# Performance work log

Measured on AMD Instinct MI355X. Metric: run time of the kernel, lower is better.

Reference implementation:

```python
import jax, jax.numpy as jnp
import numpy as np
import math

NUM_HEADS = 16
SEGMENT_SIZE = 256
DILATION_RATE = 2


def _hilbert_curve(n):
    if n == 1:
        return [(0, 0)]
    m = n // 2
    sub = _hilbert_curve(m)
    pts = [(y, x) for (x, y) in sub]
    pts += [(x, y + m) for (x, y) in sub]
    pts += [(x + m, y + m) for (x, y) in sub]
    pts += [(m - 1 - y + m, m - 1 - x) for (x, y) in sub]
    return pts


def generate_hilbert_curve_mapping(seq_len):
    grid = 2 ** int(math.ceil(math.log2(math.sqrt(seq_len))))
    pts = _hilbert_curve(grid)
    lin2hil = np.zeros(seq_len, dtype=np.int32)
    for h_idx, (x, y) in enumerate(pts[:seq_len]):
        lin = y * grid + x
        if lin < seq_len:
            lin2hil[lin] = h_idx
    return lin2hil


def setup_inputs() -> dict:
    key = jax.random.key(0)
    k1, k2, k3 = jax.random.split(key, 3)
    B, S, H = 1, 4096, 2048
    scale = H ** -0.5
    x = jax.random.normal(k1, (B, S, H), dtype=jnp.float32)
    w_qkv = jax.random.normal(k2, (3 * H, H), dtype=jnp.float32) * scale
    w_out = jax.random.normal(k3, (H, H), dtype=jnp.float32) * scale
    hilbert_map = jnp.asarray(generate_hilbert_curve_mapping(S))
    return {"x": x, "w_qkv": w_qkv, "w_out": w_out, "hilbert_map": hilbert_map}


def _kv_positions(S, seg, dil):
    # Union of per-segment dilated positions: seg_start + j*dil (< segment end).
    seg_starts = np.arange(0, S, seg)
    within = np.arange(0, seg, dil)
    return jnp.asarray((seg_starts[:, None] + within[None, :]).reshape(-1))


def reference(x, w_qkv, w_out, hilbert_map):
    B, S, H = x.shape
    nh = NUM_HEADS
    hd = H // nh
    qkv = x @ w_qkv.T                              # [B,S,3H]
    qkv = qkv.reshape(B, S, 3, nh, hd).transpose(2, 0, 3, 1, 4)  # [3,B,nh,S,hd]
    q, k, v = qkv[0], qkv[1], qkv[2]

    kv_pos = _kv_positions(S, SEGMENT_SIZE, DILATION_RATE)  # [Nk]
    gathered = hilbert_map[kv_pos]                 # Hilbert-mapped KV indices
    kg = k[:, :, gathered, :]                      # [B,nh,Nk,hd]
    vg = v[:, :, gathered, :]

    scale = 1.0 / jnp.sqrt(jnp.float32(hd))
    scores = jnp.einsum("bhmd,bhnd->bhmn", q, kg) * scale
    p = jax.nn.softmax(scores, axis=-1)
    acc = jnp.einsum("bhmn,bhnd->bhmd", p, vg)     # [B,nh,S,hd]

    # Scatter: out[:, :, hilbert_map[m], :] = acc[:, :, m, :]
    out = jnp.zeros_like(acc).at[:, :, hilbert_map, :].set(acc)
    out = out.transpose(0, 2, 1, 3).reshape(B, S, H)
    return out @ w_out.T
```

## Files before the change

kernel.cpp:

```cpp
#include <hip/hip_runtime.h>
#include <math.h>

#define S_LEN 4096
#define HID   2048
#define NH    16
#define HD    128
#define NKV   2048
#define KT    64
#define QBLK  256
#define NT    (NKV / KT)
#define QSCALE 0.12754103668587426f

typedef __attribute__((ext_vector_type(8))) _Float16 half8;
typedef __attribute__((ext_vector_type(4))) _Float16 half4;
typedef __attribute__((ext_vector_type(2))) __fp16 fp16x2;
typedef __attribute__((ext_vector_type(4))) float f32x4;
typedef __attribute__((ext_vector_type(16))) float f32x16;

#define GLB_AS __attribute__((address_space(1)))
#define LDS_AS __attribute__((address_space(3)))

#if __has_builtin(__builtin_amdgcn_exp2f)
#define EXP2(x) __builtin_amdgcn_exp2f(x)
#else
#define EXP2(x) exp2f(x)
#endif

__device__ __forceinline__ void gload16(const void* g, void* l) {
  __builtin_amdgcn_global_load_lds((GLB_AS const void*)g, (LDS_AS void*)l, 16, 0, 0);
}

__device__ __forceinline__ unsigned pkrtz(float a, float b) {
  union { fp16x2 h; unsigned u; } cv;
  cv.h = __builtin_amdgcn_cvt_pkrtz(a, b);
  return cv.u;
}

#define NX8  (S_LEN * HID / 8)
#define NW8  (3 * HID * HID / 8)
#define NO8  (HID * HID / 8)
__global__ void k_cvt_all(const float* __restrict__ x, const float* __restrict__ wq,
                          const float* __restrict__ wo, _Float16* __restrict__ x16,
                          _Float16* __restrict__ wq16, _Float16* __restrict__ wo16) {
  int i = blockIdx.x * 256 + threadIdx.x;
  const float* src; _Float16* dst; int j;
  if (i < NX8)            { src = x;  dst = x16;  j = i; }
  else if (i < NX8 + NW8) { src = wq; dst = wq16; j = i - NX8; }
  else                    { src = wo; dst = wo16; j = i - NX8 - NW8; }
  float4 a = ((const float4*)src)[2 * j];
  float4 b = ((const float4*)src)[2 * j + 1];
  half8 h;
  h[0] = (_Float16)a.x; h[1] = (_Float16)a.y; h[2] = (_Float16)a.z; h[3] = (_Float16)a.w;
  h[4] = (_Float16)b.x; h[5] = (_Float16)b.y; h[6] = (_Float16)b.z; h[7] = (_Float16)b.w;
  ((half8*)dst)[j] = h;
}

__global__ __launch_bounds__(512, 2)
void k_gemm_qkv8(const _Float16* __restrict__ A, const _Float16* __restrict__ wqkv,
                 _Float16* __restrict__ q16, const int* __restrict__ hmap,
                 char* __restrict__ kimg, char* __restrict__ vtimg)
{
  extern __shared__ __align__(16) char lds[];
  const int tid = threadIdx.x;
  const int w = tid >> 6, lane = tid & 63;
  const int l15 = lane & 15, l4 = lane >> 4;
  const int wr = w >> 2, wc = w & 3;
  const int K = HID;

  const int bid = (blockIdx.x & 7) * 32 + (blockIdx.x >> 3);
  const bool qpart = bid < 128;
  int m0, n0;
  const _Float16* B;
  if (qpart) { int b = bid;       m0 = (b >> 3) * 256; n0 = (b & 7) * 256;  B = wqkv; }
  else       { int b = bid - 128; m0 = (b >> 4) * 256; n0 = (b & 15) * 256; B = wqkv + (size_t)HID * HID; }

  const int r8 = lane >> 3;
  const int sl = (lane & 7) ^ r8;
  const _Float16* ApA[2][2];
  const _Float16* BpB[2][2];
#pragma unroll
  for (int mh = 0; mh < 2; ++mh)
#pragma unroll
    for (int L = 0; L < 2; ++L) {
      int rel = L * 128 + mh * 64 + w * 8 + r8;
      int grow = qpart ? (m0 + rel) : hmap[2 * (m0 + rel)];
      ApA[mh][L] = A + (size_t)grow * K + sl * 8;
    }
#pragma unroll
  for (int nh = 0; nh < 2; ++nh)
#pragma unroll
    for (int L = 0; L < 2; ++L) {
      int row = n0 + (L * 2 + (w >> 2)) * 64 + nh * 32 + (w & 3) * 8 + r8;
      BpB[nh][L] = B + (size_t)row * K + sl * 8;
    }

  const int sw0 = (l4 ^ (l15 & 7)) * 16;
  const int sw1 = ((4 + l4) ^ (l15 & 7)) * 16;
  const int rofs = l15 * 128;

  f32x4 acc[8][4];
#pragma unroll
  for (int i = 0; i < 8; ++i)
#pragma unroll
    for (int j = 0; j < 4; ++j) acc[i][j] = (f32x4){0.f, 0.f, 0.f, 0.f};
  half8 af[4][2], bf[2][2];

#define STG_A(MH, BUF, T)                                                       \
  do {                                                                          \
    gload16(ApA[MH][0] + (T) * 64, lds + (BUF)*65536 + (MH)*16384 + w * 1024);  \
    gload16(ApA[MH][1] + (T) * 64, lds + (BUF)*65536 + (MH)*16384 + 8192 + w * 1024); \
  } while (0)
#define STG_B(NH, BUF, T)                                                       \
  do {                                                                          \
    gload16(BpB[NH][0] + (T) * 64, lds + (BUF)*65536 + 32768 + (NH)*16384 + w * 1024); \
    gload16(BpB[NH][1] + (T) * 64, lds + (BUF)*65536 + 32768 + (NH)*16384 + 8192 + w * 1024); \
  } while (0)

#define PH(BUF, MH, NH, LA, LB, STG, WAITS)                                     \
  do {                                                                          \
    if (LA) {                                                                   \
      _Pragma("unroll")                                                         \
      for (int j = 0; j < 4; ++j) {                                             \
        af[j][0] = *(const half8*)(lds + (BUF)*65536 + (MH)*16384 + wr * 8192 + j * 2048 + rofs + sw0); \
        af[j][1] = *(const half8*)(lds + (BUF)*65536 + (MH)*16384 + wr * 8192 + j * 2048 + rofs + sw1); \
      }                                                                         \
    }                                                                           \
    if (LB) {                                                                   \
      _Pragma("unroll")                                                         \
      for (int jn = 0; jn < 2; ++jn) {                                          \
        bf[jn][0] = *(const half8*)(lds + (BUF)*65536 + 32768 + (NH)*16384 + wc * 4096 + jn * 2048 + rofs + sw0); \
        bf[jn][1] = *(const half8*)(lds + (BUF)*65536 + 32768 + (NH)*16384 + wc * 4096 + jn * 2048 + rofs + sw1); \
      }                                                                         \
    }                                                                           \
    STG;                                                                        \
    __builtin_amdgcn_s_barrier();                                               \
    __builtin_amdgcn_s_setprio(1);                                              \
    _Pragma("unroll")                                                           \
    for (int j = 0; j < 4; ++j)                                                 \
      _Pragma("unroll")                                                         \
      for (int jn = 0; jn < 2; ++jn)                                            \
        _Pragma("unroll")                                                       \
        for (int ks = 0; ks < 2; ++ks)                                          \
          acc[(MH)*4 + j][(NH)*2 + jn] = __builtin_amdgcn_mfma_f32_16x16x32_f16( \
              af[j][ks], bf[jn][ks], acc[(MH)*4 + j][(NH)*2 + jn], 0, 0, 0);    \
    __builtin_amdgcn_s_setprio(0);                                              \
    WAITS;                                                                      \
    __builtin_amdgcn_s_barrier();                                               \
  } while (0)

  STG_A(0, 0, 0); STG_B(1, 0, 0); STG_A(1, 0, 0); STG_B(0, 0, 0);
  STG_A(0, 1, 1); STG_B(1, 1, 1);
  asm volatile("s_waitcnt vmcnt(4)");
  __builtin_amdgcn_s_barrier();

  for (int i = 0; i < 15; ++i) {
    const int T1 = 2 * i + 1, T2 = 2 * i + 2, T3 = 2 * i + 3;
    PH(0, 0, 0, 1, 1, STG_A(1, 1, T1), (void)0);
    PH(0, 0, 1, 0, 1, STG_B(0, 1, T1), (void)0);
    PH(0, 1, 1, 1, 0, STG_A(0, 0, T2), (void)0);
    PH(0, 1, 0, 0, 1, STG_B(1, 0, T2), asm volatile("s_waitcnt vmcnt(4)"));
    PH(1, 0, 0, 1, 1, STG_A(1, 0, T2), (void)0);
    PH(1, 0, 1, 0, 1, STG_B(0, 0, T2), (void)0);
    PH(1, 1, 1, 1, 0, STG_A(0, 1, T3), (void)0);
    PH(1, 1, 0, 0, 1, STG_B(1, 1, T3), asm volatile("s_waitcnt vmcnt(4)"));
  }
  PH(0, 0, 0, 1, 1, STG_A(1, 1, 31), (void)0);
  PH(0, 0, 1, 0, 1, STG_B(0, 1, 31), (void)0);
  PH(0, 1, 1, 1, 0, (void)0, (void)0);
  PH(0, 1, 0, 0, 1, (void)0, asm volatile("s_waitcnt vmcnt(0)"));
  PH(1, 0, 0, 1, 1, (void)0, (void)0);
  PH(1, 0, 1, 0, 1, (void)0, (void)0);
  PH(1, 1, 1, 1, 0, (void)0, (void)0);
  PH(1, 1, 0, 0, 1, (void)0, (void)0);
#undef PH
#undef STG_A
#undef STG_B

#pragma unroll
  for (int mf = 0; mf < 8; ++mf)
#pragma unroll
    for (int nf = 0; nf < 4; ++nf)
#pragma unroll
      for (int e = 0; e < 4; ++e) {
        int row = m0 + wr * 128 + mf * 16 + l4 * 4 + e;
        int col = n0 + wc * 64 + nf * 16 + l15;
        _Float16 val = (_Float16)acc[mf][nf][e];
        if (qpart) {
          q16[(size_t)row * HID + col] = val;
        } else {
          int r = row;
          int t = r >> 6, j = r & 63;
          if (col < HID) {
            int h = col >> 7, d = col & 127;
            int off = (h * 32 + t) * 16384 + ((j * 256 + 2 * d) ^ ((j & 7) << 4));
            *(_Float16*)(kimg + off) = val;
          } else {
            int nn = col - HID;
            int h = nn >> 7, d = nn & 127;
            int off = (h * 32 + t) * 16384 + ((d * 128 + 2 * j) ^ ((d & 7) << 4));
            *(_Float16*)(vtimg + off) = val;
          }
        }
      }
}

__global__ __launch_bounds__(256)
void k_gemm_out(const _Float16* __restrict__ A, const _Float16* __restrict__ B,
                float* __restrict__ C, int M, int N, int K)
{
  __shared__ __align__(16) char Asl[16384];
  __shared__ __align__(16) char Bsl[16384];
  const int tid = threadIdx.x;
  const int w = tid >> 6, lane = tid & 63;
  const int l15 = lane & 15, l4 = lane >> 4;
  const int m0 = blockIdx.y * 128, n0 = blockIdx.x * 128;
  const int wr = w >> 1, wc = w & 1;

  const int srow  = lane >> 3;
  const int kso   = ((lane & 7) ^ srow) * 8;
  const _Float16* Ap[4];
  const _Float16* Bp[4];
#pragma unroll
  for (int q = 0; q < 4; ++q) {
    int row = m0 + 32 * w + 8 * q + srow;
    Ap[q] = A + (size_t)row * K + kso;
    Bp[q] = B + (size_t)(n0 + 32 * w + 8 * q + srow) * K + kso;
  }

  f32x4 acc[4][4];
#pragma unroll
  for (int i = 0; i < 4; ++i)
#pragma unroll
    for (int j = 0; j < 4; ++j) acc[i][j] = (f32x4){0.f, 0.f, 0.f, 0.f};

#define STAGE_T(k0)                                                  \
  do {                                                               \
    _Pragma("unroll")                                                \
    for (int q = 0; q < 4; ++q) {                                    \
      gload16(Ap[q] + (k0), Asl + (4 * w + q) * 1024 + lane * 16);   \
      gload16(Bp[q] + (k0), Bsl + (4 * w + q) * 1024 + lane * 16);   \
    }                                                                \
  } while (0)

  STAGE_T(0);
  __syncthreads();

  const int nt = K >> 6;
  for (int t = 0; t < nt; ++t) {
    half8 af[4][2], bf[4][2];
#pragma unroll
    for (int mi = 0; mi < 4; ++mi) {
      int row = wr * 64 + mi * 16 + l15;
#pragma unroll
      for (int ks = 0; ks < 2; ++ks)
        af[mi][ks] = *(const half8*)(Asl + row * 128 + (((ks * 4 + l4) ^ (row & 7)) * 16));
    }
#pragma unroll
    for (int ni = 0; ni < 4; ++ni) {
      int row = wc * 64 + ni * 16 + l15;
#pragma unroll
      for (int ks = 0; ks < 2; ++ks)
        bf[ni][ks] = *(const half8*)(Bsl + row * 128 + (((ks * 4 + l4) ^ (row & 7)) * 16));
    }
    __syncthreads();
    if (t + 1 < nt) STAGE_T((t + 1) * 64);
    __builtin_amdgcn_s_setprio(1);
#pragma unroll
    for (int mi = 0; mi < 4; ++mi)
#pragma unroll
      for (int ni = 0; ni < 4; ++ni)
#pragma unroll
        for (int ks = 0; ks < 2; ++ks)
          acc[mi][ni] = __builtin_amdgcn_mfma_f32_16x16x32_f16(af[mi][ks], bf[ni][ks], acc[mi][ni], 0, 0, 0);
    __builtin_amdgcn_s_setprio(0);
    __syncthreads();
  }
#undef STAGE_T

  const int rbase = m0 + wr * 64 + l4 * 4;
  const int cbase = n0 + wc * 64 + l15;
#pragma unroll
  for (int mi = 0; mi < 4; ++mi)
#pragma unroll
    for (int ni = 0; ni < 4; ++ni)
#pragma unroll
      for (int e = 0; e < 4; ++e)
        C[(size_t)(rbase + mi * 16 + e) * N + cbase + ni * 16] = acc[mi][ni][e];
}

__global__ __launch_bounds__(512, 2)
void k_attn9(const _Float16* __restrict__ qmat, const char* __restrict__ kimg,
             const char* __restrict__ vtimg, const int* __restrict__ hmap,
             _Float16* __restrict__ att)
{
  extern __shared__ __align__(16) char lds[];
  const int tid = threadIdx.x;
  const int w = tid >> 6, lane = tid & 63;
  const int l31 = lane & 31;
  const bool hi = (lane >> 5) != 0;
  const int hib = hi ? 1 : 0;
  const int work = (blockIdx.x & 7) * 32 + (blockIdx.x >> 3);
  const int h  = work >> 4;
  const int q0 = (work & 15) * QBLK;

  half8 qf[8];
  {
    const int qrow = q0 + w * 32 + l31;
    const _Float16* qb = qmat + (size_t)qrow * HID + h * HD + hib * 8;
    const _Float16 qs = (_Float16)QSCALE;
#pragma unroll
    for (int dk = 0; dk < 8; ++dk) {
      half8 v = *(const half8*)(qb + 16 * dk);
#pragma unroll
      for (int q = 0; q < 8; ++q) v[q] *= qs;
      qf[dk] = v;
    }
  }

  const int swz = (l31 & 7) << 4;
  int koff[4], voff[4];
#pragma unroll
  for (int i = 0; i < 4; ++i) {
    koff[i] = l31 * 256 + ((i * 32 + hib * 16) ^ swz);
    voff[i] = 16384 + l31 * 128 + ((i * 32 + hib * 16) ^ swz);
  }

  const char* kbase = kimg  + (size_t)h * NT * 16384;
  const char* vbase = vtimg + (size_t)h * NT * 16384;

  f32x16 acc[4];
#pragma unroll
  for (int dt = 0; dt < 4; ++dt)
#pragma unroll
    for (int r = 0; r < 16; ++r) acc[dt][r] = 0.f;
  float lsum = 0.f;

#define STAGE(buf, t)                                                          \
  do {                                                                         \
    const char* ks_ = kbase + (size_t)(t) * 16384;                             \
    const char* vs_ = vbase + (size_t)(t) * 16384;                             \
    char* d_ = lds + (buf) * 32768;                                            \
    gload16(ks_ + w * 1024 + lane * 16,          d_ + w * 1024);               \
    gload16(ks_ + (8 + w) * 1024 + lane * 16,    d_ + (8 + w) * 1024);         \
    gload16(vs_ + w * 1024 + lane * 16,          d_ + 16384 + w * 1024);       \
    gload16(vs_ + (8 + w) * 1024 + lane * 16,    d_ + 16384 + (8 + w) * 1024); \
  } while (0)

#define SM_HALF(S, PPK)                                                        \
  do {                                                                         \
    float p_[16];                                                              \
    _Pragma("unroll")                                                          \
    for (int r = 0; r < 16; ++r) { p_[r] = EXP2((S)[r]); lsum += p_[r]; }      \
    _Pragma("unroll")                                                          \
    for (int rq = 0; rq < 4; ++rq)                                             \
      _Pragma("unroll")                                                        \
      for (int h2 = 0; h2 < 2; ++h2)                                           \
        PPK[rq][h2] = pkrtz(p_[4 * rq + 2 * h2], p_[4 * rq + 2 * h2 + 1]);     \
  } while (0)

#define PV_HALF(PPK, KSB, CUR)                                                 \
  do {                                                                         \
    _Pragma("unroll")                                                          \
    for (int k1 = 0; k1 < 2; ++k1) {                                           \
      unsigned send0 = hi ? PPK[2 * k1][0]     : PPK[2 * k1 + 1][0];           \
      unsigned send1 = hi ? PPK[2 * k1][1]     : PPK[2 * k1 + 1][1];           \
      unsigned recv0 = (unsigned)__shfl_xor((int)send0, 32);                   \
      unsigned recv1 = (unsigned)__shfl_xor((int)send1, 32);                   \
      unsigned self0 = hi ? PPK[2 * k1 + 1][0] : PPK[2 * k1][0];               \
      unsigned self1 = hi ? PPK[2 * k1 + 1][1] : PPK[2 * k1][1];               \
      union { unsigned u[4]; half8 hv; } pf;                                   \
      pf.u[0] = hi ? recv0 : self0;                                            \
      pf.u[1] = hi ? recv1 : self1;                                            \
      pf.u[2] = hi ? self0 : recv0;                                            \
      pf.u[3] = hi ? self1 : recv1;                                            \
      __builtin_amdgcn_s_setprio(1);                                           \
      _Pragma("unroll")                                                        \
      for (int dt = 0; dt < 4; ++dt) {                                         \
        half8 vf = *(const half8*)(lds + voff[(KSB) + k1] +                    \
                    ((CUR) * 32768 + dt * 4096));                              \
        acc[dt] = __builtin_amdgcn_mfma_f32_32x32x16_f16(vf, pf.hv, acc[dt], 0, 0, 0); \
      }                                                                        \
      __builtin_amdgcn_s_setprio(0);                                           \
    }                                                                          \
  } while (0)

#define QK_HALF(S, JT, CUR)                                                    \
  do {                                                                         \
    _Pragma("unroll")                                                          \
    for (int r = 0; r < 16; ++r) (S)[r] = 0.f;                                 \
    __builtin_amdgcn_s_setprio(1);                                             \
    _Pragma("unroll")                                                          \
    for (int dk = 0; dk < 8; ++dk) {                                           \
      half8 kf = *(const half8*)(lds + koff[dk & 3] +                          \
                  ((CUR) * 32768 + (JT) * 8192 + (dk >> 2) * 128));            \
      (S) = __builtin_amdgcn_mfma_f32_32x32x16_f16(kf, qf[dk], (S), 0, 0, 0);  \
    }                                                                          \
    __builtin_amdgcn_s_setprio(0);                                             \
  } while (0)

#define TILE(CUR, T)                                                           \
  do {                                                                         \
    if ((T) + 1 < NT) STAGE((CUR) ^ 1, (T) + 1);                               \
    f32x16 sA, sB;                                                             \
    QK_HALF(sA, 0, CUR);                                                       \
    QK_HALF(sB, 1, CUR);                                                       \
    unsigned PA[4][2], PB[4][2];                                               \
    SM_HALF(sA, PA);                                                           \
    PV_HALF(PA, 0, CUR);                                                       \
    SM_HALF(sB, PB);                                                           \
    PV_HALF(PB, 2, CUR);                                                       \
    asm volatile("s_waitcnt vmcnt(0)");                                        \
    __syncthreads();                                                           \
  } while (0)

  STAGE(0, 0);
  asm volatile("s_waitcnt vmcnt(0)");
  __syncthreads();

  for (int t = 0; t < NT; t += 2) {
    TILE(0, t);
    TILE(1, t + 1);
  }
#undef TILE
#undef QK_HALF
#undef PV_HALF
#undef SM_HALF
#undef STAGE

  float lt = lsum + __shfl_xor(lsum, 32);
  const float rl = 1.0f / lt;
  const int qrow = q0 + w * 32 + l31;
  const int srow = hmap[qrow];
  _Float16* ob = att + (size_t)srow * HID + h * HD;
#pragma unroll
  for (int dt = 0; dt < 4; ++dt)
#pragma unroll
    for (int rq = 0; rq < 4; ++rq) {
      const int d0 = dt * 32 + 8 * rq + 4 * hib;
      half4 o;
      o[0] = (_Float16)(acc[dt][4 * rq + 0] * rl);
      o[1] = (_Float16)(acc[dt][4 * rq + 1] * rl);
      o[2] = (_Float16)(acc[dt][4 * rq + 2] * rl);
      o[3] = (_Float16)(acc[dt][4 * rq + 3] * rl);
      *(half4*)(ob + d0) = o;
    }
}

extern "C" void kernel_launch(void* const* d_in, const int* in_sizes, int n_in,
                              void* d_out, int out_size, void* d_ws, size_t ws_size,
                              hipStream_t stream)
{
  const float* x     = (const float*)d_in[0];
  const float* w_qkv = (const float*)d_in[1];
  const float* w_out = (const float*)d_in[2];
  const int*   hmap  = (const int*)d_in[3];
  float* out = (float*)d_out;

  char* ws = (char*)d_ws;
  _Float16* x16    = (_Float16*)ws;
  _Float16* att16  = (_Float16*)ws;                              ws += (size_t)S_LEN * HID * 2;
  _Float16* wqkv16 = (_Float16*)ws;                              ws += (size_t)3 * HID * HID * 2;
  _Float16* wout16 = (_Float16*)ws;                              ws += (size_t)HID * HID * 2;
  _Float16* q16    = (_Float16*)ws;                              ws += (size_t)S_LEN * HID * 2;
  char* kimg  = ws;                                              ws += (size_t)NH * NT * 16384;
  char* vtimg = ws;

  k_cvt_all<<<(NX8 + NW8 + NO8 + 255) / 256, 256, 0, stream>>>(x, w_qkv, w_out,
                                                               x16, wqkv16, wout16);

  k_gemm_qkv8<<<256, 512, 131072, stream>>>(x16, wqkv16, q16, hmap, kimg, vtimg);

  k_attn9<<<NH * (S_LEN / QBLK), 512, 65536, stream>>>(q16, kimg, vtimg, hmap, att16);

  dim3 go(HID / 128, S_LEN / 128);
  k_gemm_out<<<go, 256, 0, stream>>>(att16, wout16, out, S_LEN, HID, HID);
}
```

Measured before the change: 209.1 us.

## Rewrite output GEMM as 8-wave 256x128 tile kernel with phased double-buffered pipeline

Replaces the 256-thread 128x128 output projection GEMM with a 512-thread kernel computing 256x128 tiles over 256 blocks. It double-buffers A/B tiles in dynamic LDS and splits each K-step into eight phases that interleave global-to-LDS loads with MFMA work, using raw barriers and explicit vmcnt waits. Block IDs are remapped to group work for L2 locality. The aim is better latency hiding and one-wave-per-CU occupancy, at the cost of more LDS, a hand-tuned schedule that is fragile to get right, and a hardcoded problem size.

```diff
diff --git a/kernel.cpp b/kernel.cpp
--- a/kernel.cpp
+++ b/kernel.cpp
@@ -204,88 +204,120 @@
       }
 }
 
-__global__ __launch_bounds__(256)
-void k_gemm_out(const _Float16* __restrict__ A, const _Float16* __restrict__ B,
-                float* __restrict__ C, int M, int N, int K)
+__global__ __launch_bounds__(512, 2)
+void k_gemm_out8(const _Float16* __restrict__ A, const _Float16* __restrict__ B,
+                 float* __restrict__ C)
 {
-  __shared__ __align__(16) char Asl[16384];
-  __shared__ __align__(16) char Bsl[16384];
+  extern __shared__ __align__(16) char lds[];
   const int tid = threadIdx.x;
   const int w = tid >> 6, lane = tid & 63;
   const int l15 = lane & 15, l4 = lane >> 4;
-  const int m0 = blockIdx.y * 128, n0 = blockIdx.x * 128;
-  const int wr = w >> 1, wc = w & 1;
-
-  const int srow  = lane >> 3;
-  const int kso   = ((lane & 7) ^ srow) * 8;
-  const _Float16* Ap[4];
-  const _Float16* Bp[4];
-#pragma unroll
-  for (int q = 0; q < 4; ++q) {
-    int row = m0 + 32 * w + 8 * q + srow;
-    Ap[q] = A + (size_t)row * K + kso;
-    Bp[q] = B + (size_t)(n0 + 32 * w + 8 * q + srow) * K + kso;
+  const int wr = w >> 2, wc = w & 3;
+  const int K = HID;
+
+  const int bid = (blockIdx.x & 7) * 32 + (blockIdx.x >> 3);
+  const int m0 = (bid >> 4) * 256;
+  const int n0 = (bid & 15) * 128;
+
+  const int r8 = lane >> 3;
+  const int sl = (lane & 7) ^ r8;
+  const _Float16* ApA[2][2];
+  const _Float16* Bp[2];
+#pragma unroll
+  for (int mh = 0; mh < 2; ++mh)
+#pragma unroll
+    for (int L = 0; L < 2; ++L) {
+      int rel = L * 128 + mh * 64 + w * 8 + r8;
+      ApA[mh][L] = A + (size_t)(m0 + rel) * K + sl * 8;
+    }
+#pragma unroll
+  for (int nh = 0; nh < 2; ++nh) {
+    int row = n0 + (w >> 1) * 32 + nh * 16 + (w & 1) * 8 + r8;
+    Bp[nh] = B + (size_t)row * K + sl * 8;
   }
 
-  f32x4 acc[4][4];
-#pragma unroll
-  for (int i = 0; i < 4; ++i)
-#pragma unroll
-    for (int j = 0; j < 4; ++j) acc[i][j] = (f32x4){0.f, 0.f, 0.f, 0.f};
-
-#define STAGE_T(k0)                                                  \
-  do {                                                               \
-    _Pragma("unroll")                                                \
-    for (int q = 0; q < 4; ++q) {                                    \
-      gload16(Ap[q] + (k0), Asl + (4 * w + q) * 1024 + lane * 16);   \
-      gload16(Bp[q] + (k0), Bsl + (4 * w + q) * 1024 + lane * 16);   \
-    }                                                                \
-  } while (0)
-
-  STAGE_T(0);
-  __syncthreads();
-
-  const int nt = K >> 6;
-  for (int t = 0; t < nt; ++t) {
-    half8 af[4][2], bf[4][2];
-#pragma unroll
-    for (int mi = 0; mi < 4; ++mi) {
-      int row = wr * 64 + mi * 16 + l15;
-#pragma unroll
-      for (int ks = 0; ks < 2; ++ks)
-        af[mi][ks] = *(const half8*)(Asl + row * 128 + (((ks * 4 + l4) ^ (row & 7)) * 16));
-    }
-#pragma unroll
-    for (int ni = 0; ni < 4; ++ni) {
-      int row = wc * 64 + ni * 16 + l15;
-#pragma unroll
-      for (int ks = 0; ks < 2; ++ks)
-        bf[ni][ks] = *(const half8*)(Bsl + row * 128 + (((ks * 4 + l4) ^ (row & 7)) * 16));
-    }
-    __syncthreads();
-    if (t + 1 < nt) STAGE_T((t + 1) * 64);
-    __builtin_amdgcn_s_setprio(1);
-#pragma unroll
-    for (int mi = 0; mi < 4; ++mi)
-#pragma unroll
-      for (int ni = 0; ni < 4; ++ni)
-#pragma unroll
-        for (int ks = 0; ks < 2; ++ks)
-          acc[mi][ni] = __builtin_amdgcn_mfma_f32_16x16x32_f16(af[mi][ks], bf[ni][ks], acc[mi][ni], 0, 0, 0);
-    __builtin_amdgcn_s_setprio(0);
-    __syncthreads();
+  const int sw0 = (l4 ^ (l15 & 7)) * 16;
+  const int sw1 = ((4 + l4) ^ (l15 & 7)) * 16;
+  const int rofs = l15 * 128;
+
+  f32x4 acc[8][2];
+#pragma unroll
+  for (int i = 0; i < 8; ++i)
+#pragma unroll
+    for (int j = 0; j < 2; ++j) acc[i][j] = (f32x4){0.f, 0.f, 0.f, 0.f};
+  half8 af[4][2], bf[2];
+
+#define STG_A(MH, BUF, T)                                                       \
+  do {                                                                          \
+    gload16(ApA[MH][0] + (T) * 64, lds + (BUF)*49152 + (MH)*16384 + w * 1024);  \
+    gload16(ApA[MH][1] + (T) * 64, lds + (BUF)*49152 + (MH)*16384 + 8192 + w * 1024); \
+  } while (0)
+#define STG_B(NH, BUF, T)                                                       \
+  gload16(Bp[NH] + (T) * 64, lds + (BUF)*49152 + 32768 + (NH)*8192 + w * 1024)
+
+#define PH(BUF, MH, NH, LA, STG, WAITS)                                         \
+  do {                                                                          \
+    if (LA) {                                                                   \
+      _Pragma("unroll")                                                         \
+      for (int j = 0; j < 4; ++j) {                                             \
+        af[j][0] = *(const half8*)(lds + (BUF)*49152 + (MH)*16384 + wr * 8192 + j * 2048 + rofs + sw0); \
+        af[j][1] = *(const half8*)(lds + (BUF)*49152 + (MH)*16384 + wr * 8192 + j * 2048 + rofs + sw1); \
+      }                                                                         \
+    }                                                                           \
+    bf[0] = *(const half8*)(lds + (BUF)*49152 + 32768 + (NH)*8192 + wc * 2048 + rofs + sw0); \
+    bf[1] = *(const half8*)(lds + (BUF)*49152 + 32768 + (NH)*8192 + wc * 2048 + rofs + sw1); \
+    STG;                                                                        \
+    __builtin_amdgcn_s_barrier();                                               \
+    __builtin_amdgcn_s_setprio(1);                                              \
+    _Pragma("unroll")                                                           \
+    for (int j = 0; j < 4; ++j)                                                 \
+      _Pragma("unroll")                                                         \
+      for (int ks = 0; ks < 2; ++ks)                                            \
+        acc[(MH)*4 + j][NH] = __builtin_amdgcn_mfma_f32_16x16x32_f16(           \
+            af[j][ks], bf[ks], acc[(MH)*4 + j][NH], 0, 0, 0);                   \
+    __builtin_amdgcn_s_setprio(0);                                              \
+    WAITS;                                                                      \
+    __builtin_amdgcn_s_barrier();                                               \
+  } while (0)
+
+  STG_A(0, 0, 0); STG_B(1, 0, 0); STG_A(1, 0, 0); STG_B(0, 0, 0);
+  STG_A(0, 1, 1); STG_B(1, 1, 1);
+  asm volatile("s_waitcnt vmcnt(3)");
+  __builtin_amdgcn_s_barrier();
+
+  for (int i = 0; i < 15; ++i) {
+    const int T1 = 2 * i + 1, T2 = 2 * i + 2, T3 = 2 * i + 3;
+    PH(0, 0, 0, 1, STG_A(1, 1, T1), (void)0);
+    PH(0, 0, 1, 0, STG_B(0, 1, T1), (void)0);
+    PH(0, 1, 1, 1, STG_A(0, 0, T2), (void)0);
+    PH(0, 1, 0, 0, STG_B(1, 0, T2), asm volatile("s_waitcnt vmcnt(3)"));
+    PH(1, 0, 0, 1, STG_A(1, 0, T2), (void)0);
+    PH(1, 0, 1, 0, STG_B(0, 0, T2), (void)0);
+    PH(1, 1, 1, 1, STG_A(0, 1, T3), (void)0);
+    PH(1, 1, 0, 0, STG_B(1, 1, T3), asm volatile("s_waitcnt vmcnt(3)"));
   }
-#undef STAGE_T
-
-  const int rbase = m0 + wr * 64 + l4 * 4;
-  const int cbase = n0 + wc * 64 + l15;
-#pragma unroll
-  for (int mi = 0; mi < 4; ++mi)
-#pragma unroll
-    for (int ni = 0; ni < 4; ++ni)
-#pragma unroll
-      for (int e = 0; e < 4; ++e)
-        C[(size_t)(rbase + mi * 16 + e) * N + cbase + ni * 16] = acc[mi][ni][e];
+  PH(0, 0, 0, 1, STG_A(1, 1, 31), (void)0);
+  PH(0, 0, 1, 0, STG_B(0, 1, 31), (void)0);
+  PH(0, 1, 1, 1, (void)0, (void)0);
+  PH(0, 1, 0, 0, (void)0, asm volatile("s_waitcnt vmcnt(0)"));
+  PH(1, 0, 0, 1, (void)0, (void)0);
+  PH(1, 0, 1, 0, (void)0, (void)0);
+  PH(1, 1, 1, 1, (void)0, (void)0);
+  PH(1, 1, 0, 0, (void)0, (void)0);
+#undef PH
+#undef STG_A
+#undef STG_B
+
+#pragma unroll
+  for (int mf = 0; mf < 8; ++mf)
+#pragma unroll
+    for (int nf = 0; nf < 2; ++nf)
+#pragma unroll
+      for (int e = 0; e < 4; ++e) {
+        int row = m0 + wr * 128 + mf * 16 + l4 * 4 + e;
+        int col = n0 + wc * 32 + nf * 16 + l15;
+        C[(size_t)row * HID + col] = acc[mf][nf][e];
+      }
 }
 
 __global__ __launch_bounds__(512, 2)
@@ -472,6 +504,5 @@
 
   k_attn9<<<NH * (S_LEN / QBLK), 512, 65536, stream>>>(q16, kimg, vtimg, hmap, att16);
 
-  dim3 go(HID / 128, S_LEN / 128);
-  k_gemm_out<<<go, 256, 0, stream>>>(att16, wout16, out, S_LEN, HID, HID);
-}
+  k_gemm_out8<<<256, 512, 98304, stream>>>(att16, wout16, out);
+}
```

Result: no change. 208.1 us, median of 2 (-0.5%).
